# Optimization experiments

Measured on AMD Instinct MI355X. Metric: run time of the kernel, lower is better.

Reference implementation:

```python
import jax, jax.numpy as jnp
import numpy as np

PC_RANGE = (-51.2, -51.2, -3.0, 51.2, 51.2, 1.0)
OUT = 3   # roi_align_size
SR = 2    # fixed sampling ratio (approximates mmcv adaptive sampling_ratio=0)


def roi_align_rotated(fm, rois_b, cx, cy, w, h, angle):
    """mmcv-style RoIAlignRotated, aligned=True, spatial_scale=1, clockwise=True.
    fm: [B,C,H,W]; rois_b int [N]; cx,cy,w,h,angle float [N]. Returns [N,C,OUT,OUT]."""
    B, C, H, W = fm.shape
    fm_hwc = jnp.transpose(fm, (0, 2, 3, 1))  # [B,H,W,C] for channel-last gather
    cx = cx - 0.5  # aligned=True pixel-center offset
    cy = cy - 0.5
    theta = -angle  # clockwise=True
    cos_t, sin_t = jnp.cos(theta), jnp.sin(theta)
    bin_h = h / OUT
    bin_w = w / OUT
    ph = jnp.arange(OUT, dtype=fm.dtype)
    sg = (jnp.arange(SR, dtype=fm.dtype) + 0.5) / SR
    # local (un-rotated) sample coords, [N, OUT, SR]
    yy = -h[:, None, None] / 2 + (ph[None, :, None] + sg[None, None, :]) * bin_h[:, None, None]
    xx = -w[:, None, None] / 2 + (ph[None, :, None] + sg[None, None, :]) * bin_w[:, None, None]
    # broadcast to [N, OUT(ph), OUT(pw), SR(iy), SR(ix)]
    yy = yy[:, :, None, :, None]
    xx = xx[:, None, :, None, :]
    c = cos_t[:, None, None, None, None]
    s = sin_t[:, None, None, None, None]
    y = yy * c - xx * s + cy[:, None, None, None, None]
    x = yy * s + xx * c + cx[:, None, None, None, None]
    N = cx.shape[0]
    P = OUT * OUT * SR * SR
    y = y.reshape(N, P)
    x = x.reshape(N, P)
    valid = (y > -1.0) & (y < H) & (x > -1.0) & (x < W)
    y = jnp.clip(y, 0.0, H - 1)
    x = jnp.clip(x, 0.0, W - 1)
    y0 = jnp.minimum(jnp.floor(y).astype(jnp.int32), H - 1)
    x0 = jnp.minimum(jnp.floor(x).astype(jnp.int32), W - 1)
    y1 = jnp.minimum(y0 + 1, H - 1)
    x1 = jnp.minimum(x0 + 1, W - 1)
    ly = y - y0
    lx = x - x0
    hy, hx = 1.0 - ly, 1.0 - lx
    bi = rois_b[:, None].astype(jnp.int32)
    v00 = fm_hwc[bi, y0, x0]  # [N,P,C]
    v01 = fm_hwc[bi, y0, x1]
    v10 = fm_hwc[bi, y1, x0]
    v11 = fm_hwc[bi, y1, x1]
    val = (hy * hx)[..., None] * v00 + (hy * lx)[..., None] * v01 \
        + (ly * hx)[..., None] * v10 + (ly * lx)[..., None] * v11
    val = val * valid[..., None].astype(fm.dtype)
    val = val.reshape(N, OUT, OUT, SR * SR, C).mean(axis=3)  # average over samples
    return jnp.transpose(val, (0, 3, 1, 2))  # [N,C,OUT,OUT]


def fc2(x, w1, w2):
    # two Conv1d(k=1, bias=False) + ReLU == two bias-free linears + ReLU
    return jax.nn.relu(jax.nn.relu(x @ w1.T) @ w2.T)


def setup_inputs() -> dict:
    key = jax.random.key(0)
    ks = jax.random.split(key, 20)
    B, C, H, W, N = 4, 256, 256, 256, 2048
    F = OUT * OUT * C  # 2304
    D = 256            # n_fc_neurons
    fm = jax.random.normal(ks[0], (B, C, H, W), jnp.float32)
    u = jax.random.uniform(ks[1], (N, 7), jnp.float32)
    boxes = jnp.stack([
        u[:, 0] * 90.0 - 45.0,        # x in [-45,45] m
        u[:, 1] * 90.0 - 45.0,        # y
        u[:, 2] * 2.0 - 2.0,          # z
        u[:, 3] * 4.5 + 1.5,          # h
        u[:, 4] * 4.5 + 1.5,          # w (roi height in pixels)
        u[:, 5] * 4.5 + 1.5,          # l (roi width in pixels)
        u[:, 6] * 2.0 * np.pi - np.pi  # yaw
    ], axis=1)
    bidx = jax.random.randint(ks[2], (N,), 0, B, dtype=jnp.int32)
    def mkw(k, o, i):
        return jax.random.normal(k, (o, i), jnp.float32) * np.float32(1.0 / np.sqrt(i))
    return {
        'feature_map': fm, 'boxes': boxes, 'batch_idx': bidx,
        'w_sh1': mkw(ks[3], D, F), 'w_sh2': mkw(ks[4], D, D),
        'w_cls1': mkw(ks[5], D, D), 'w_cls2': mkw(ks[6], D, D),
        'w_cls3': mkw(ks[7], 1, D), 'b_cls3': jnp.zeros((1,), jnp.float32),
        'w_iou1': mkw(ks[8], D, D), 'w_iou2': mkw(ks[9], D, D),
        'w_iou3': mkw(ks[10], 1, D), 'b_iou3': jnp.zeros((1,), jnp.float32),
        'w_reg1': mkw(ks[11], D, D), 'w_reg2': mkw(ks[12], D, D),
        'w_reg3': mkw(ks[13], 7, D) * np.float32(0.001), 'b_reg3': jnp.zeros((7,), jnp.float32),
    }


def reference(feature_map, boxes, batch_idx,
              w_sh1, w_sh2,
              w_cls1, w_cls2, w_cls3, b_cls3,
              w_iou1, w_iou2, w_iou3, b_iou3,
              w_reg1, w_reg2, w_reg3, b_reg3):
    H, W = feature_map.shape[2], feature_map.shape[3]
    gw = (PC_RANGE[3] - PC_RANGE[0]) / W
    gh = (PC_RANGE[4] - PC_RANGE[1]) / H
    cx = (boxes[:, 0] - PC_RANGE[0]) / gw
    cy = (boxes[:, 1] - PC_RANGE[1]) / gh
    rw = boxes[:, 5] / gw  # enlarge_ratio = 1
    rh = boxes[:, 4] / gh
    ang = boxes[:, 6]
    pooled = roi_align_rotated(feature_map, batch_idx, cx, cy, rw, rh, ang)  # [N,C,3,3]
    N, C = pooled.shape[0], pooled.shape[1]
    # flatten(2).permute(0,2,1).flatten(1): bin-major, channel-minor
    x = jnp.transpose(pooled.reshape(N, C, OUT * OUT), (0, 2, 1)).reshape(N, OUT * OUT * C)
    sh = fc2(x, w_sh1, w_sh2)
    rcnn_cls = fc2(sh, w_cls1, w_cls2) @ w_cls3.T + b_cls3
    rcnn_iou = fc2(sh, w_iou1, w_iou2) @ w_iou3.T + b_iou3
    rcnn_reg = fc2(sh, w_reg1, w_reg2) @ w_reg3.T + b_reg3
    return rcnn_cls, rcnn_iou, rcnn_reg
```

## Files before the change

### kernel.cpp

```cpp
#include <hip/hip_runtime.h>
#include <hip/hip_fp16.h>

typedef float f4v __attribute__((ext_vector_type(4)));
typedef _Float16 h4 __attribute__((ext_vector_type(4)));
typedef _Float16 h8 __attribute__((ext_vector_type(8)));

#define NROI 2048
#define NCH  256
#define MAPH 256
#define MAPW 256
#define HWSZ (MAPH*MAPW)
#define FDIM 2304
#define MN   (2048*256)

#define O_SH1 0
#define O_SH2 589824
#define O_C1  655360
#define O_C2  720896
#define O_I1  786432
#define O_I2  851968
#define O_R1  917504
#define O_R2  983040
#define WTOT  1048576

__global__ __launch_bounds__(256) void convert_w_kernel(
    const float* __restrict__ s1, const float* __restrict__ s2,
    const float* __restrict__ c1, const float* __restrict__ c2,
    const float* __restrict__ i1, const float* __restrict__ i2,
    const float* __restrict__ r1, const float* __restrict__ r2,
    __half* __restrict__ wbuf)
{
    const int b = blockIdx.x, t = threadIdx.x;
    const float* src;
    int base;
    if (b < 1152) { src = s1 + (size_t)b*512; base = b*512; }
    else {
        int j  = (b - 1152) >> 7;
        int lb = (b - 1152) & 127;
        switch (j) {
            case 0: src = s2; break; case 1: src = c1; break;
            case 2: src = c2; break; case 3: src = i1; break;
            case 4: src = i2; break; case 5: src = r1; break;
            default: src = r2; break;
        }
        src += (size_t)lb*512;
        base = 589824 + (b - 1152)*512;
    }
    float2 v = *(const float2*)(src + t*2);
    *(__half2*)(wbuf + base + t*2) = __floats2half2_rn(v.x, v.y);
}

__global__ __launch_bounds__(256) void transpose_kernel(
    const float* __restrict__ fm, __half* __restrict__ hwc)
{
    __shared__ float tile[64*65];
    const int tid = threadIdx.x;
    const int x0 = blockIdx.x * 64, c0 = blockIdx.y * 64;
    const int bz = blockIdx.z;
    const int b = bz >> 8, y = bz & 255;

    const int lane = tid & 63, cg = tid >> 6;
    const float* src = fm + (((size_t)b*NCH + c0 + cg*16)*MAPH + y)*MAPW + x0 + lane;
    #pragma unroll
    for (int i = 0; i < 16; i++)
        tile[(cg*16 + i)*65 + lane] = src[(size_t)i * HWSZ];
    __syncthreads();

    __half* dst = hwc + (((size_t)b*MAPH + y)*MAPW + x0)*NCH + c0;
    const int c2 = (tid & 31) * 2;
    const int xb = tid >> 5;
    #pragma unroll
    for (int k = 0; k < 8; k++) {
        int x = xb + k*8;
        float f0 = tile[c2*65 + x];
        float f1 = tile[(c2+1)*65 + x];
        *(__half2*)(dst + (size_t)x*NCH + c2) = __floats2half2_rn(f0, f1);
    }
}

__global__ __launch_bounds__(256) void roi_hwc_kernel(
    const __half* __restrict__ hwc, const float* __restrict__ boxes,
    const int* __restrict__ bidx, __half* __restrict__ xout)
{
    const int tid = threadIdx.x;
    const int r   = tid >> 7;
    const int lt  = tid & 127;
    const int n   = blockIdx.x * 2 + r;

    __shared__ float sw[2][4][36];
    __shared__ int   soff[2][4][36];
    __shared__ int   sb[2];

    if (lt < 36) {
        float b0 = boxes[n*7+0], b1 = boxes[n*7+1];
        float b4 = boxes[n*7+4], b5 = boxes[n*7+5], b6 = boxes[n*7+6];
        float cx = (b0 + 51.2f) / 0.4f - 0.5f;
        float cy = (b1 + 51.2f) / 0.4f - 0.5f;
        float w  = b5 / 0.4f;
        float h  = b4 / 0.4f;
        float th = -b6;
        float ct = cosf(th), st = sinf(th);
        float binh = h / 3.0f, binw = w / 3.0f;
        int s  = lt;
        int ph = s / 12, pw = (s % 12) / 4, sy = (s % 4) / 2, sx = s & 1;
        float sgy = ((float)sy + 0.5f) * 0.5f;
        float sgx = ((float)sx + 0.5f) * 0.5f;
        float yy  = -h*0.5f + ((float)ph + sgy) * binh;
        float xxl = -w*0.5f + ((float)pw + sgx) * binw;
        float y = yy*ct - xxl*st + cy;
        float x = yy*st + xxl*ct + cx;
        bool valid = (y > -1.0f) && (y < 256.0f) && (x > -1.0f) && (x < 256.0f);
        y = fminf(fmaxf(y, 0.0f), 255.0f);
        x = fminf(fmaxf(x, 0.0f), 255.0f);
        int y0 = (int)floorf(y); if (y0 > 255) y0 = 255;
        int x0 = (int)floorf(x); if (x0 > 255) x0 = 255;
        int y1 = min(y0+1, 255), x1 = min(x0+1, 255);
        float ly = y - (float)y0, lx = x - (float)x0;
        float hy = 1.0f - ly, hx = 1.0f - lx;
        float v = valid ? 0.25f : 0.0f;
        sw[r][0][s] = hy*hx*v; sw[r][1][s] = hy*lx*v;
        sw[r][2][s] = ly*hx*v; sw[r][3][s] = ly*lx*v;
        soff[r][0][s] = (y0*MAPW + x0)*NCH;
        soff[r][1][s] = (y0*MAPW + x1)*NCH;
        soff[r][2][s] = (y1*MAPW + x0)*NCH;
        soff[r][3][s] = (y1*MAPW + x1)*NCH;
    }
    if (lt == 0) sb[r] = bidx[n];
    __syncthreads();

    const __half* base = hwc + (size_t)sb[r]*(HWSZ*NCH) + lt*2;
    __half* xo = xout + (size_t)n*FDIM + lt*2;

    #pragma unroll 3
    for (int pp = 0; pp < 9; pp++) {
        float ax = 0.f, ay = 0.f;
        #pragma unroll
        for (int q = 0; q < 4; q++) {
            int s = pp*4 + q;
            #pragma unroll
            for (int c = 0; c < 4; c++) {
                __half2 v = *(const __half2*)(base + soff[r][c][s]);
                float2 f = __half22float2(v);
                float wgt = sw[r][c][s];
                ax += wgt * f.x;
                ay += wgt * f.y;
            }
        }
        *(__half2*)(xo + pp*NCH) = __floats2half2_rn(ax, ay);
    }
}

struct PtrsH {
    const __half* A[3];
    const __half* W[3];
    void* C[3];
};

__device__ inline h8 ldsH8(const _Float16* p) {
    h4 lo = *(const h4*)p;
    h4 hi = *(const h4*)(p + 4);
    return __builtin_shufflevector(lo, hi, 0,1,2,3,4,5,6,7);
}

template<bool RELU, bool SPLITK, bool OUTH>
__global__ __launch_bounds__(256) void gemm_h_kernel(PtrsH p, int M, int N, int K, int kChunk)
{
    __shared__ _Float16 As[64*40];
    __shared__ _Float16 Ws[64*40];
    const int z = blockIdx.z;
    const _Float16* A; const _Float16* W; void* C;
    int k0, k1;
    if (SPLITK) {
        A = (const _Float16*)p.A[0]; W = (const _Float16*)p.W[0];
        k0 = z * kChunk; k1 = k0 + kChunk;
        C = (char*)p.C[0] + (size_t)z * M * N * 4;
    } else {
        A = (const _Float16*)p.A[z]; W = (const _Float16*)p.W[z]; C = p.C[z];
        k0 = 0; k1 = K;
    }
    const int tid = threadIdx.x;
    const int m0 = blockIdx.x * 64, n0 = blockIdx.y * 64;
    const int srow = tid >> 2, skc = (tid & 3) * 8;
    const _Float16* Ald = A + (size_t)(m0 + srow) * K + k0 + skc;
    const _Float16* Wld = W + (size_t)(n0 + srow) * K + k0 + skc;
    const int wv = tid >> 6, lane = tid & 63;
    const int quad = lane >> 4, mr = lane & 15;

    f4v acc[4] = {};
    h8 aR = *(const h8*)Ald;
    h8 wR = *(const h8*)Wld;

    for (int kt = k0; kt < k1; kt += 32) {
        __syncthreads();
        *(h4*)&As[srow*40 + skc]     = __builtin_shufflevector(aR, aR, 0,1,2,3);
        *(h4*)&As[srow*40 + skc + 4] = __builtin_shufflevector(aR, aR, 4,5,6,7);
        *(h4*)&Ws[srow*40 + skc]     = __builtin_shufflevector(wR, wR, 0,1,2,3);
        *(h4*)&Ws[srow*40 + skc + 4] = __builtin_shufflevector(wR, wR, 4,5,6,7);
        __syncthreads();
        if (kt + 32 < k1) {
            Ald += 32; Wld += 32;
            aR = *(const h8*)Ald;
            wR = *(const h8*)Wld;
        }
        h8 af = ldsH8(&As[(wv*16 + mr)*40 + quad*8]);
        #pragma unroll
        for (int j = 0; j < 4; j++) {
            h8 bf = ldsH8(&Ws[(j*16 + mr)*40 + quad*8]);
            acc[j] = __builtin_amdgcn_mfma_f32_16x16x32_f16(af, bf, acc[j], 0, 0, 0);
        }
    }

    const int orow = m0 + wv*16 + quad*4;
    #pragma unroll
    for (int j = 0; j < 4; j++) {
        int col = n0 + j*16 + mr;
        #pragma unroll
        for (int rr = 0; rr < 4; rr++) {
            float v = acc[j][rr];
            if (RELU) v = fmaxf(v, 0.0f);
            if (OUTH) ((__half*)C)[(size_t)(orow + rr) * N + col] = __float2half(v);
            else      ((float*)C)[(size_t)(orow + rr) * N + col] = v;
        }
    }
}

__global__ __launch_bounds__(256) void reduce_relu_h_kernel(
    const float* __restrict__ pin, __half* __restrict__ hout)
{
    int i = blockIdx.x * 256 + threadIdx.x;
    const f4v* p4 = (const f4v*)pin;
    f4v a = p4[i];
    a += p4[i + MN/4];
    a += p4[i + 2*(MN/4)];
    a += p4[i + 3*(MN/4)];
    h4 o;
    #pragma unroll
    for (int j = 0; j < 4; j++) o[j] = (_Float16)fmaxf(a[j], 0.0f);
    *(h4*)(hout + (size_t)i*4) = o;
}

__global__ __launch_bounds__(256) void heads_kernel(
    const float* __restrict__ c2, const float* __restrict__ i2, const float* __restrict__ r2,
    const float* __restrict__ wc3, const float* __restrict__ bc3,
    const float* __restrict__ wi3, const float* __restrict__ bi3,
    const float* __restrict__ wr3, const float* __restrict__ br3,
    float* __restrict__ out)
{
    const int lane = threadIdx.x & 63;
    const int wv   = threadIdx.x >> 6;
    const int n    = blockIdx.x * 4 + wv;
    const float* cr = c2 + (size_t)n*256;
    const float* ir = i2 + (size_t)n*256;
    const float* rr = r2 + (size_t)n*256;
    float vc = 0.0f, vi = 0.0f, vr[7] = {};
    #pragma unroll
    for (int j = 0; j < 4; j++) {
        int k = lane + j*64;
        float cv = cr[k], iv = ir[k], rv = rr[k];
        vc += cv * wc3[k];
        vi += iv * wi3[k];
        #pragma unroll
        for (int t = 0; t < 7; t++) vr[t] += rv * wr3[t*256 + k];
    }
    #pragma unroll
    for (int off = 32; off > 0; off >>= 1) {
        vc += __shfl_down(vc, off, 64);
        vi += __shfl_down(vi, off, 64);
        #pragma unroll
        for (int t = 0; t < 7; t++) vr[t] += __shfl_down(vr[t], off, 64);
    }
    if (lane == 0) {
        out[n]        = vc + bc3[0];
        out[2048 + n] = vi + bi3[0];
        #pragma unroll
        for (int t = 0; t < 7; t++) out[4096 + n*7 + t] = vr[t] + br3[t];
    }
}

extern "C" void kernel_launch(void* const* d_in, const int* in_sizes, int n_in,
                              void* d_out, int out_size, void* d_ws, size_t ws_size,
                              hipStream_t stream)
{
    const float* fm    = (const float*)d_in[0];
    const float* boxes = (const float*)d_in[1];
    const int*   bidx  = (const int*)d_in[2];
    const float* w_sh1 = (const float*)d_in[3];
    const float* w_sh2 = (const float*)d_in[4];
    const float* w_c1  = (const float*)d_in[5];
    const float* w_c2  = (const float*)d_in[6];
    const float* w_c3  = (const float*)d_in[7];
    const float* b_c3  = (const float*)d_in[8];
    const float* w_i1  = (const float*)d_in[9];
    const float* w_i2  = (const float*)d_in[10];
    const float* w_i3  = (const float*)d_in[11];
    const float* b_i3  = (const float*)d_in[12];
    const float* w_r1  = (const float*)d_in[13];
    const float* w_r2  = (const float*)d_in[14];
    const float* w_r3  = (const float*)d_in[15];
    const float* b_r3  = (const float*)d_in[16];
    float* out = (float*)d_out;

    char* base = (char*)d_ws;
    __half* hwc  = (__half*)base;
    __half* xh   = (__half*)(base + (size_t)4*NCH*HWSZ*2);
    __half* h1h  = (__half*)((char*)xh + (size_t)NROI*FDIM*2);
    __half* shh  = (__half*)((char*)h1h + (size_t)MN*2);
    __half* b1c  = (__half*)((char*)shh + (size_t)MN*2);
    __half* b1i  = b1c + MN;
    __half* b1r  = b1i + MN;
    float*  b2c  = (float*)((char*)b1c + (size_t)3*MN*2);
    float*  b2i  = b2c + MN;
    float*  b2r  = b2i + MN;
    float*  part = (float*)((char*)b2c + (size_t)3*MN*4);
    __half* wbuf = (__half*)((char*)part + (size_t)4*MN*4);

    convert_w_kernel<<<2048, 256, 0, stream>>>(w_sh1, w_sh2, w_c1, w_c2,
                                               w_i1, w_i2, w_r1, w_r2, wbuf);
    transpose_kernel<<<dim3(MAPW/64, NCH/64, 4*MAPH), 256, 0, stream>>>(fm, hwc);
    roi_hwc_kernel<<<NROI/2, 256, 0, stream>>>(hwc, boxes, bidx, xh);

    PtrsH g1;
    g1.A[0]=g1.A[1]=g1.A[2]=xh;
    g1.W[0]=g1.W[1]=g1.W[2]=wbuf + O_SH1;
    g1.C[0]=g1.C[1]=g1.C[2]=part;
    gemm_h_kernel<false,true,false><<<dim3(32,4,4), 256, 0, stream>>>(g1, 2048, 256, 2304, 576);

    reduce_relu_h_kernel<<<MN/4/256, 256, 0, stream>>>(part, h1h);

    PtrsH g2;
    g2.A[0]=g2.A[1]=g2.A[2]=h1h;
    g2.W[0]=g2.W[1]=g2.W[2]=wbuf + O_SH2;
    g2.C[0]=g2.C[1]=g2.C[2]=shh;
    gemm_h_kernel<true,false,true><<<dim3(32,4,1), 256, 0, stream>>>(g2, 2048, 256, 256, 0);

    PtrsH g3;
    g3.A[0]=g3.A[1]=g3.A[2]=shh;
    g3.W[0]=wbuf + O_C1; g3.W[1]=wbuf + O_I1; g3.W[2]=wbuf + O_R1;
    g3.C[0]=b1c; g3.C[1]=b1i; g3.C[2]=b1r;
    gemm_h_kernel<true,false,true><<<dim3(32,4,3), 256, 0, stream>>>(g3, 2048, 256, 256, 0);

    PtrsH g4;
    g4.A[0]=b1c; g4.A[1]=b1i; g4.A[2]=b1r;
    g4.W[0]=wbuf + O_C2; g4.W[1]=wbuf + O_I2; g4.W[2]=wbuf + O_R2;
    g4.C[0]=b2c; g4.C[1]=b2i; g4.C[2]=b2r;
    gemm_h_kernel<true,false,false><<<dim3(32,4,3), 256, 0, stream>>>(g4, 2048, 256, 256, 0);

    heads_kernel<<<NROI/4, 256, 0, stream>>>(b2c, b2i, b2r,
                                             w_c3, b_c3, w_i3, b_i3, w_r3, b_r3, out);
}
```

Measured before the change: 474.5 us.

## Widen transpose tiles with fp16 LDS staging and vectorize RoI gathers

The NCHW-to-NHWC transpose now handles 128x128 tiles. Each thread reads float4 rows and converts them to fp16 while staging in shared memory, then writes 8-byte h4 vectors. The rotated RoI gather changes from half2 to h4 loads, with the 9 bins split across two 64-lane groups per RoI. Both changes aim to cut memory transaction count and raise bytes per access on the bandwidth-bound transpose and gather stages. The risks are more shared-memory bank conflicts from the strided fp16 stores and uneven bin work between the two groups (5 vs 4 bins).

```diff
diff --git a/kernel.cpp b/kernel.cpp
--- a/kernel.cpp
+++ b/kernel.cpp
@@ -21,7 +21,6 @@
 #define O_I2  851968
 #define O_R1  917504
 #define O_R2  983040
-#define WTOT  1048576
 
 __global__ __launch_bounds__(256) void convert_w_kernel(
     const float* __restrict__ s1, const float* __restrict__ s2,
@@ -50,31 +49,40 @@
     *(__half2*)(wbuf + base + t*2) = __floats2half2_rn(v.x, v.y);
 }
 
+#define TP 136
+
 __global__ __launch_bounds__(256) void transpose_kernel(
     const float* __restrict__ fm, __half* __restrict__ hwc)
 {
-    __shared__ float tile[64*65];
+    __shared__ _Float16 tile[128 * TP];
     const int tid = threadIdx.x;
-    const int x0 = blockIdx.x * 64, c0 = blockIdx.y * 64;
+    const int x0 = blockIdx.x * 128, c0 = blockIdx.y * 128;
     const int bz = blockIdx.z;
     const int b = bz >> 8, y = bz & 255;
 
-    const int lane = tid & 63, cg = tid >> 6;
-    const float* src = fm + (((size_t)b*NCH + c0 + cg*16)*MAPH + y)*MAPW + x0 + lane;
-    #pragma unroll
-    for (int i = 0; i < 16; i++)
-        tile[(cg*16 + i)*65 + lane] = src[(size_t)i * HWSZ];
+    const int c    = tid & 127;
+    const int half = tid >> 7;
+    const float* src = fm + (((size_t)b*NCH + c0 + c)*MAPH + y)*MAPW + x0 + half*64;
+
+    #pragma unroll
+    for (int j = 0; j < 16; j++) {
+        f4v v = *(const f4v*)(src + j*4);
+        const int xl = half*64 + j*4;
+        tile[(xl+0)*TP + c] = (_Float16)v[0];
+        tile[(xl+1)*TP + c] = (_Float16)v[1];
+        tile[(xl+2)*TP + c] = (_Float16)v[2];
+        tile[(xl+3)*TP + c] = (_Float16)v[3];
+    }
     __syncthreads();
 
-    __half* dst = hwc + (((size_t)b*MAPH + y)*MAPW + x0)*NCH + c0;
-    const int c2 = (tid & 31) * 2;
+    const int cq = tid & 31;
     const int xb = tid >> 5;
-    #pragma unroll
-    for (int k = 0; k < 8; k++) {
-        int x = xb + k*8;
-        float f0 = tile[c2*65 + x];
-        float f1 = tile[(c2+1)*65 + x];
-        *(__half2*)(dst + (size_t)x*NCH + c2) = __floats2half2_rn(f0, f1);
+    __half* dst = hwc + (((size_t)b*MAPH + y)*MAPW + x0)*NCH + c0 + cq*4;
+    #pragma unroll
+    for (int it = 0; it < 16; it++) {
+        int x = xb + it*8;
+        h4 v = *(const h4*)&tile[x*TP + cq*4];
+        *(h4*)(dst + (size_t)x*NCH) = v;
     }
 }
 
@@ -82,10 +90,12 @@
     const __half* __restrict__ hwc, const float* __restrict__ boxes,
     const int* __restrict__ bidx, __half* __restrict__ xout)
 {
-    const int tid = threadIdx.x;
-    const int r   = tid >> 7;
-    const int lt  = tid & 127;
-    const int n   = blockIdx.x * 2 + r;
+    const int tid  = threadIdx.x;
+    const int r    = tid >> 7;
+    const int lt   = tid & 127;
+    const int wq   = lt >> 6;
+    const int lane = lt & 63;
+    const int n    = blockIdx.x * 2 + r;
 
     __shared__ float sw[2][4][36];
     __shared__ int   soff[2][4][36];
@@ -128,25 +138,26 @@
     if (lt == 0) sb[r] = bidx[n];
     __syncthreads();
 
-    const __half* base = hwc + (size_t)sb[r]*(HWSZ*NCH) + lt*2;
-    __half* xo = xout + (size_t)n*FDIM + lt*2;
-
-    #pragma unroll 3
-    for (int pp = 0; pp < 9; pp++) {
-        float ax = 0.f, ay = 0.f;
+    const __half* base = hwc + (size_t)sb[r]*(HWSZ*NCH) + lane*4;
+    __half* xo = xout + (size_t)n*FDIM + lane*4;
+
+    for (int pp = wq; pp < 9; pp += 2) {
+        float a0 = 0.f, a1 = 0.f, a2 = 0.f, a3 = 0.f;
         #pragma unroll
         for (int q = 0; q < 4; q++) {
             int s = pp*4 + q;
             #pragma unroll
-            for (int c = 0; c < 4; c++) {
-                __half2 v = *(const __half2*)(base + soff[r][c][s]);
-                float2 f = __half22float2(v);
-                float wgt = sw[r][c][s];
-                ax += wgt * f.x;
-                ay += wgt * f.y;
+            for (int cc = 0; cc < 4; cc++) {
+                h4 v = *(const h4*)(base + soff[r][cc][s]);
+                float wgt = sw[r][cc][s];
+                a0 += wgt * (float)v[0];
+                a1 += wgt * (float)v[1];
+                a2 += wgt * (float)v[2];
+                a3 += wgt * (float)v[3];
             }
         }
-        *(__half2*)(xo + pp*NCH) = __floats2half2_rn(ax, ay);
+        h4 o; o[0]=(_Float16)a0; o[1]=(_Float16)a1; o[2]=(_Float16)a2; o[3]=(_Float16)a3;
+        *(h4*)(xo + pp*NCH) = o;
     }
 }
 
@@ -316,7 +327,7 @@
 
     convert_w_kernel<<<2048, 256, 0, stream>>>(w_sh1, w_sh2, w_c1, w_c2,
                                                w_i1, w_i2, w_r1, w_r2, wbuf);
-    transpose_kernel<<<dim3(MAPW/64, NCH/64, 4*MAPH), 256, 0, stream>>>(fm, hwc);
+    transpose_kernel<<<dim3(2, 2, 4*MAPH), 256, 0, stream>>>(fm, hwc);
     roi_hwc_kernel<<<NROI/2, 256, 0, stream>>>(hwc, boxes, bidx, xh);
 
     PtrsH g1;
```

Result: no change. 471.6 us (-0.6%).
